# Kernel optimization log

Measured on AMD Instinct MI355X. Metric: run time of the kernel, lower is better.

The kernel has to match this reference:

```python
import jax, jax.numpy as jnp
import numpy as np

EPS = 1e-5
DILATIONS = (1, 2, 1, 2, 1, 2, 1, 2)   # 4 blocks x 2 layers, kernel_size=2
GCN_AT = {1: 0, 5: 1}                  # ChebConv applied before layers 1 and 5
N_NODES, T_IN, N_EDGES = 20000, 13, 200000
RC, DC, SC, EC, HORIZON = 32, 32, 256, 512, 12


def conv_1x1(x, W, b):
    # x: [N,C,T], W: [O,C] -> [N,O,T]
    return jnp.einsum('oc,nct->not', W, x) + b[None, :, None]


def conv_k2(x, W, b, d):
    # dilated conv, kernel=2, dilation=d. x: [N,C,T], W: [O,C,2] -> [N,O,T-d]
    y = jnp.einsum('oc,nct->not', W[:, :, 0], x[:, :, :-d]) \
        + jnp.einsum('oc,nct->not', W[:, :, 1], x[:, :, d:])
    return y + b[None, :, None]


def _batchnorm(x):
    # BatchNorm2d (train mode, gamma=1, beta=0); per-channel stats over (N, F=1, T)
    m = jnp.mean(x, axis=(0, 2), keepdims=True)
    v = jnp.var(x, axis=(0, 2), keepdims=True)
    return (x - m) / jnp.sqrt(v + EPS)


def _cheb(xf, edge_index, edge_attr, W0, W1, b):
    n = xf.shape[0]
    row, col = edge_index[0], edge_index[1]
    w = jnp.where(row == col, 0.0, edge_attr)               # remove_self_loops
    deg = jax.ops.segment_sum(w, row, num_segments=n)
    dinv = jnp.where(deg > 0, 1.0 / jnp.sqrt(jnp.where(deg > 0, deg, 1.0)), 0.0)
    norm = dinv[row] * w * dinv[col]                        # [E]
    tx1 = -jax.ops.segment_sum(norm[:, None] * xf[row], col, num_segments=n)
    return xf @ W0 + tx1 @ W1 + b


def _forward(x, edge_index, edge_attr, start_W, start_b, filter_W, filter_b,
             gate_W, gate_b, skip_W, skip_b, gcn0_W0, gcn0_W1, gcn0_b,
             gcn1_W0, gcn1_W1, gcn1_b, end1_W, end1_b, end2_W, end2_b):
    # instance norm over time (use_norm=True); means is detached in torch
    means = jax.lax.stop_gradient(jnp.mean(x, axis=1, keepdims=True))   # [N,1,1]
    xc = x - means
    stdev = jnp.sqrt(jnp.var(xc, axis=1, keepdims=True) + EPS)
    xc = xc / stdev
    h = xc[:, :, 0][:, None, :]                  # [N,1,13]  (F=1 dim folded away)
    h = conv_1x1(h, start_W, start_b)            # [N,32,13]; T == receptive_field, no pad
    gcns = ((gcn0_W0, gcn0_W1, gcn0_b), (gcn1_W0, gcn1_W1, gcn1_b))
    skip = None
    for i, d in enumerate(DILATIONS):
        if i in GCN_AT:
            n, c, t = h.shape
            W0, W1, b = gcns[GCN_AT[i]]
            h = _cheb(h.reshape(n, c * t), edge_index, edge_attr, W0, W1, b).reshape(n, c, t)
        residual = h
        f = jnp.tanh(conv_k2(residual, filter_W[i], filter_b[i], d))
        g = jax.nn.sigmoid(conv_k2(residual, gate_W[i], gate_b[i], d))
        h = f * g                                 # [N,32,t-d]
        s = conv_1x1(h, skip_W[i], skip_b[i])     # [N,256,t-d]
        skip = s if skip is None else s + skip[:, :, -s.shape[2]:]
        h = h + residual[:, :, -h.shape[2]:]      # residual add (residual_conv unused in source)
        h = _batchnorm(h)
    out = jax.nn.relu(skip)                       # [N,256,1]
    out = conv_1x1(out, end1_W, end1_b)           # [N,512,1]
    out = conv_1x1(out, end2_W, end2_b)           # [N,12,1]
    return out * stdev + means                    # de-normalize; broadcasts over horizon


def setup_inputs() -> dict:
    key = jax.random.key(0)
    ks = iter(jax.random.split(key, 32))
    def w(shape, scale=0.1):
        return jax.random.normal(next(ks), shape, dtype=jnp.float32) * scale
    return {
        'x': jax.random.normal(next(ks), (N_NODES, T_IN, 1), dtype=jnp.float32),
        'edge_index': jax.random.randint(next(ks), (2, N_EDGES), 0, N_NODES),
        'edge_attr': jax.random.uniform(next(ks), (N_EDGES,), dtype=jnp.float32),
        'start_W': w((RC, 1)), 'start_b': w((RC,)),
        'filter_W': w((8, DC, RC, 2)), 'filter_b': w((8, DC)),
        'gate_W': w((8, DC, RC, 2)), 'gate_b': w((8, DC)),
        'skip_W': w((8, SC, DC)), 'skip_b': w((8, SC)),
        'gcn0_W0': w((384, 384), 0.05), 'gcn0_W1': w((384, 384), 0.05), 'gcn0_b': w((384,)),
        'gcn1_W0': w((192, 192), 0.05), 'gcn1_W1': w((192, 192), 0.05), 'gcn1_b': w((192,)),
        'end1_W': w((EC, SC)), 'end1_b': w((EC,)),
        'end2_W': w((HORIZON, EC)), 'end2_b': w((HORIZON,)),
    }


def reference(x, edge_index, edge_attr, start_W, start_b, filter_W, filter_b,
              gate_W, gate_b, skip_W, skip_b, gcn0_W0, gcn0_W1, gcn0_b,
              gcn1_W0, gcn1_W1, gcn1_b, end1_W, end1_b, end2_W, end2_b):
    return _forward(x, edge_index, edge_attr, start_W, start_b, filter_W, filter_b,
                    gate_W, gate_b, skip_W, skip_b, gcn0_W0, gcn0_W1, gcn0_b,
                    gcn1_W0, gcn1_W1, gcn1_b, end1_W, end1_b, end2_W, end2_b)
```

## Files before the change

kernel.cpp:

```cpp
#include <hip/hip_runtime.h>
#include <math.h>

#define NN 20000
#define NE 200000
#define TT 13
#define NBLK 79

typedef short bf16x8 __attribute__((ext_vector_type(8)));
typedef float f32x4 __attribute__((ext_vector_type(4)));

__device__ inline unsigned short f2bf(float f){
  union{float f; unsigned u;} v; v.f = f;
  unsigned r = v.u + 0x7fffu + ((v.u >> 16) & 1u);
  return (unsigned short)(r >> 16);
}
__device__ inline float bf2f(unsigned short h){
  union{unsigned u; float f;} v; v.u = ((unsigned)h) << 16; return v.f;
}
__device__ inline float fsig(float x){ return __builtin_amdgcn_rcpf(1.f + __expf(-x)); }
__device__ inline float ftanh(float x){ return 2.f*__builtin_amdgcn_rcpf(1.f + __expf(-2.f*x)) - 1.f; }

__device__ inline void d_prepw2(const float* W0, const float* W1, const float* b,
    unsigned short* Wt, float* bPerm, int F, int Kp, int T, int idx){
  if(idx >= F*Kp) return;
  int o = idx / Kp, k = idx - o*Kp;
  int to = o >> 5, co = o & 31; int fout = co*T + to;
  int ki = (k < F) ? k : k - F;
  int ti = ki >> 5, ci = ki & 31; int fin = ci*T + ti;
  float v = (k < F) ? W0[fin*F + fout] : W1[fin*F + fout];
  Wt[idx] = f2bf(v);
  if(k == 0) bPerm[o] = b[fout];
}
__device__ inline void d_prep2(const float* sW, const float* sb,
    unsigned short* Bwt, float* b2, int idx){
  if(idx >= 65536) return;
  int sOut = idx >> 8; int ic = idx & 255; int i = ic >> 5; int c = ic & 31;
  Bwt[idx] = f2bf(sW[i*8192 + sOut*32 + c]);
  if(idx < 256){
    float acc = 0.f;
    for(int ll = 0; ll < 8; ll++) acc += sb[ll*256 + idx];
    b2[idx] = acc;
  }
}
__device__ inline void d_comb(const float* e1W, const float* e1b,
    const float* e2W, const float* e2b, float* Wc, float* bc, int idx){
  if(idx >= 12*256) return;
  int k = idx >> 8, c = idx & 255;
  float acc = 0.f;
  for(int o = 0; o < 512; o++) acc += e2W[k*512+o]*e1W[o*256+c];
  Wc[idx] = acc;
  if(c == 0){
    float b = e2b[k];
    for(int o = 0; o < 512; o++) b += e2W[k*512+o]*e1b[o];
    bc[k] = b;
  }
}
__device__ inline void d_prepg(const float* fW, const float* fb,
    const float* gW, const float* gb, unsigned short* Wfrag, float* Bfrag, int idx){
  if(idx < 8*8*64*8){
    int j = idx & 7; int lane = (idx >> 3) & 63; int chunk = (idx >> 9) & 7; int layer = idx >> 12;
    int fg = chunk >> 2; int q = (chunk >> 1) & 1; int i = chunk & 1;
    int quad = lane >> 4, tcol = lane & 15;
    int cout = 16*i + tcol, cin = quad*8 + j;
    const float* W = fg ? gW : fW;
    Wfrag[idx] = f2bf(W[layer*2048 + cout*64 + cin*2 + q]);
  }
  if(idx < 8*64*4){
    int r = idx & 3; int lane = (idx >> 2) & 63; int layer = idx >> 8;
    int tcol = lane & 15;
    float v;
    if(r == 0)      v = fb[layer*32 + tcol];
    else if(r == 1) v = fb[layer*32 + 16 + tcol];
    else if(r == 2) v = gb[layer*32 + tcol];
    else            v = gb[layer*32 + 16 + tcol];
    Bfrag[idx] = v;
  }
}
__global__ __launch_bounds__(256) void k_prepall(
    const float* g0W0, const float* g0W1, const float* g0b,
    const float* g1W0, const float* g1W1, const float* g1b,
    const float* sW, const float* sb,
    const float* e1W, const float* e1b, const float* e2W, const float* e2b,
    const float* fW, const float* fb, const float* gW, const float* gb,
    unsigned short* Wt0, float* bP0, unsigned short* Wt1, float* bP1,
    unsigned short* Bwt, float* bias2, float* Wc, float* bc,
    unsigned short* Wfrag, float* Bfrag){
  int b = blockIdx.x, t = threadIdx.x;
  if(b < 1152)       d_prepw2(g0W0, g0W1, g0b, Wt0, bP0, 384, 768, 12, b*256 + t);
  else if(b < 1440)  d_prepw2(g1W0, g1W1, g1b, Wt1, bP1, 192, 384, 6, (b-1152)*256 + t);
  else if(b < 1696)  d_prep2(sW, sb, Bwt, bias2, (b-1440)*256 + t);
  else if(b < 1708)  d_comb(e1W, e1b, e2W, e2b, Wc, bc, (b-1696)*256 + t);
  else               d_prepg(fW, fb, gW, gb, Wfrag, Bfrag, (b-1708)*256 + t);
}

__global__ __launch_bounds__(256) void k_deg(const int* __restrict__ ei,
    const float* __restrict__ ea, float* __restrict__ deg){
  int e = blockIdx.x*256 + threadIdx.x;
  if(e >= NE) return;
  int r = ei[e], c = ei[NE+e];
  float w = (r==c) ? 0.f : ea[e];
  if(w != 0.f) atomicAdd(&deg[r], w);
}

__global__ __launch_bounds__(256) void k_dinv(float* __restrict__ deg){
  int n = blockIdx.x*256 + threadIdx.x;
  if(n >= NN) return;
  float d = deg[n];
  deg[n] = (d > 0.f) ? rsqrtf(d) : 0.f;
}

__global__ __launch_bounds__(256) void k_normcount(const int* __restrict__ ei,
    const float* __restrict__ ea, const float* __restrict__ dinv,
    float* __restrict__ nrm, int* __restrict__ cnt){
  int e = blockIdx.x*256 + threadIdx.x;
  if(e >= NE) return;
  int r = ei[e], c = ei[NE+e];
  float w = (r==c) ? 0.f : ea[e];
  float nv = dinv[r]*w*dinv[c];
  nrm[e] = nv;
  if(nv != 0.f) atomicAdd(&cnt[c], 1);
}

__global__ __launch_bounds__(256) void k_scanA(const int* __restrict__ cnt, int* __restrict__ bsum){
  int i = blockIdx.x*256 + threadIdx.x;
  int l = threadIdx.x & 63, w = threadIdx.x >> 6;
  int v = (i < NN) ? cnt[i] : 0;
#pragma unroll
  for(int off = 1; off < 64; off <<= 1) v += __shfl_xor(v, off);
  __shared__ int ws4[4];
  if(l == 0) ws4[w] = v;
  __syncthreads();
  if(threadIdx.x == 0) bsum[blockIdx.x] = ws4[0]+ws4[1]+ws4[2]+ws4[3];
}

__global__ __launch_bounds__(128) void k_scanB(const int* __restrict__ bsum, int* __restrict__ bbase){
  __shared__ int buf[128];
  int t = threadIdx.x;
  int v = (t < NBLK) ? bsum[t] : 0;
  buf[t] = v; __syncthreads();
  for(int off = 1; off < 128; off <<= 1){
    int u = (t >= off) ? buf[t-off] : 0;
    __syncthreads();
    buf[t] += u;
    __syncthreads();
  }
  if(t < NBLK) bbase[t] = buf[t] - v;
  if(t == NBLK-1) bbase[NBLK] = buf[t];
}

__global__ __launch_bounds__(256) void k_scanC(const int* __restrict__ cnt,
    const int* __restrict__ bbase, int* __restrict__ rowptr, int* __restrict__ woff){
  int i = blockIdx.x*256 + threadIdx.x;
  int t = threadIdx.x, l = t & 63, w = t >> 6;
  int v = (i < NN) ? cnt[i] : 0;
  int x = v;
#pragma unroll
  for(int off = 1; off < 64; off <<= 1){
    int u = __shfl_up(x, off);
    if(l >= off) x += u;
  }
  __shared__ int wt[4];
  if(l == 63) wt[w] = x;
  __syncthreads();
  int wo = 0;
  for(int k = 0; k < w; k++) wo += wt[k];
  int excl = bbase[blockIdx.x] + wo + x - v;
  if(i < NN){ rowptr[i] = excl; woff[i] = excl; }
  if(i == 0) rowptr[NN] = bbase[NBLK];
}

__global__ __launch_bounds__(256) void k_place(const float* __restrict__ nrm,
    const int* __restrict__ ei, int* __restrict__ woff,
    int* __restrict__ rowArr, float* __restrict__ nrmArr){
  int e = blockIdx.x*256 + threadIdx.x;
  if(e >= NE) return;
  float nv = nrm[e];
  if(nv == 0.f) return;
  int c = ei[NE+e];
  int pos = atomicAdd(&woff[c], 1);
  rowArr[pos] = ei[e];
  nrmArr[pos] = nv;
}

__global__ __launch_bounds__(64) void k_bnfold(const float* __restrict__ in, float* __restrict__ out){
  int t = threadIdx.x;
  float s = 0.f;
#pragma unroll
  for(int b = 0; b < 16; b++) s += in[b*64 + t];
  out[t] = s;
}

__global__ __launch_bounds__(256) void k_cvtbn2(const unsigned short* __restrict__ h,
    const float* __restrict__ bn, float cntInv, unsigned short* __restrict__ A,
    int F, int Kp){
  int idx = blockIdx.x*256 + threadIdx.x;
  int half = F >> 1;
  if(idx >= NN*half) return;
  int n = idx / half, r = idx - n*half;
  int k0 = 2*r; int c0 = k0 & 31;
  unsigned u = *(const unsigned*)(h + (size_t)n*F + k0);
  float m0 = bn[c0]*cntInv, m1 = bn[c0+1]*cntInv;
  float i0 = rsqrtf(bn[32+c0]*cntInv - m0*m0 + 1e-5f);
  float i1 = rsqrtf(bn[32+c0+1]*cntInv - m1*m1 + 1e-5f);
  float v0 = (bf2f((unsigned short)(u & 0xffffu)) - m0)*i0;
  float v1 = (bf2f((unsigned short)(u >> 16)) - m1)*i1;
  unsigned outw = (unsigned)f2bf(v0) | ((unsigned)f2bf(v1) << 16);
  *(unsigned*)(A + (size_t)n*Kp + k0) = outw;
}

__global__ void k_gather2(const unsigned short* __restrict__ Acat, int Kp, int F, int F2,
    const int* __restrict__ rowArr, const float* __restrict__ nrmArr,
    const int* __restrict__ rowptr, unsigned short* __restrict__ dst){
  int node = blockIdx.x;
  int f2 = threadIdx.x;
  int beg = rowptr[node], end = rowptr[node+1];
  __shared__ int srow[64];
  __shared__ float snrm[64];
  float a0 = 0.f, a1 = 0.f;
  for(int base = beg; base < end; base += 64){
    int m = end - base; if(m > 64) m = 64;
    __syncthreads();
    if(threadIdx.x < m){ srow[threadIdx.x] = rowArr[base+threadIdx.x]; snrm[threadIdx.x] = nrmArr[base+threadIdx.x]; }
    __syncthreads();
    if(f2 < F2){
      for(int j = 0; j < m; j++){
        unsigned u = *(const unsigned*)(Acat + (size_t)srow[j]*Kp + 2*f2);
        float nv = snrm[j];
        a0 += nv*bf2f((unsigned short)(u & 0xffffu));
        a1 += nv*bf2f((unsigned short)(u >> 16));
      }
    }
  }
  if(f2 < F2){
    unsigned outw = (unsigned)f2bf(-a0) | ((unsigned)f2bf(-a1) << 16);
    *(unsigned*)(dst + (size_t)node*Kp + F + 2*f2) = outw;
  }
}

template<bool BOUT>
__global__ __launch_bounds__(256) void k_gemm_bf16(const unsigned short* __restrict__ A,
    const unsigned short* __restrict__ Bt, const float* __restrict__ bias,
    void* __restrict__ Cv, int M, int N, int K){
  __shared__ unsigned short As[128*32];
  __shared__ unsigned short Bs[64*32];
  int tid = threadIdx.x;
  int w = tid >> 6, l = tid & 63, quad = l >> 4, tcol = l & 15;
  int m0 = blockIdx.x*128, n0 = blockIdx.y*64;
  int rw = (w & 1)*64, cw = (w >> 1)*32;
  int sr = tid >> 2, sc = (tid & 3)*8;
  f32x4 acc[4][2];
#pragma unroll
  for(int i = 0; i < 4; i++)
#pragma unroll
    for(int j = 0; j < 2; j++) acc[i][j] = (f32x4){0.f,0.f,0.f,0.f};
  for(int k0 = 0; k0 < K; k0 += 32){
    uint4 a0 = *(const uint4*)(A + (size_t)(m0 + sr)*K + k0 + sc);
    uint4 a1 = *(const uint4*)(A + (size_t)(m0 + 64 + sr)*K + k0 + sc);
    uint4 b0 = *(const uint4*)(Bt + (size_t)(n0 + sr)*K + k0 + sc);
    __syncthreads();
    *(uint4*)(As + sr*32 + sc) = a0;
    *(uint4*)(As + (64+sr)*32 + sc) = a1;
    *(uint4*)(Bs + sr*32 + sc) = b0;
    __syncthreads();
    bf16x8 av[4], bv[2];
#pragma unroll
    for(int i = 0; i < 4; i++) av[i] = *(const bf16x8*)(As + (rw + 16*i + tcol)*32 + quad*8);
#pragma unroll
    for(int j = 0; j < 2; j++) bv[j] = *(const bf16x8*)(Bs + (cw + 16*j + tcol)*32 + quad*8);
#pragma unroll
    for(int i = 0; i < 4; i++)
#pragma unroll
      for(int j = 0; j < 2; j++)
        acc[i][j] = __builtin_amdgcn_mfma_f32_16x16x32_bf16(av[i], bv[j], acc[i][j], 0, 0, 0);
  }
#pragma unroll
  for(int i = 0; i < 4; i++){
#pragma unroll
    for(int j = 0; j < 2; j++){
      int col = n0 + cw + 16*j + tcol;
      float bb = bias[col];
#pragma unroll
      for(int r = 0; r < 4; r++){
        int row = m0 + rw + 16*i + quad*4 + r;
        if(row < M){
          float o = acc[i][j][r] + bb;
          if(BOUT) ((unsigned short*)Cv)[(size_t)row*N + col] = f2bf(o);
          else ((float*)Cv)[(size_t)row*N + col] = o;
        }
      }
    }
  }
}

__global__ __launch_bounds__(256,3) void k_fused0nb(
    const float* __restrict__ x, const float* __restrict__ startW, const float* __restrict__ startb,
    const unsigned short* __restrict__ Wfrag, const float* __restrict__ Bfrag,
    unsigned short* __restrict__ glcat, unsigned short* __restrict__ hOut,
    float* __restrict__ stdev, float* __restrict__ means,
    float* __restrict__ bnstats){
  __shared__ float xs[40][14];
  __shared__ float swl[32], sbl[32];
  __shared__ unsigned short bufB[40*12*40];
  __shared__ float bnred[64];
  int tid = threadIdx.x;
  int w = tid >> 6, l = tid & 63, quad = l >> 4, tcol = l & 15;
  int base = blockIdx.x*40;
  for(int j = tid; j < 520; j += 256){ int n = j/13, t = j - n*13; xs[n][t] = x[(size_t)(base+n)*13 + t]; }
  if(tid < 32){ swl[tid] = startW[tid]; sbl[tid] = startb[tid]; }
  if(tid < 64) bnred[tid] = 0.f;
  __syncthreads();
  if(tid < 40){
    float s = 0.f;
#pragma unroll
    for(int t = 0; t < 13; t++) s += xs[tid][t];
    float m = s*(1.0f/13.f);
    float s2 = 0.f;
#pragma unroll
    for(int t = 0; t < 13; t++){ float d = xs[tid][t]-m; s2 += d*d; }
    float sd = sqrtf(s2*(1.0f/13.f) + 1e-5f);
    float inv = 1.0f/sd;
    means[base+tid] = m; stdev[base+tid] = sd;
#pragma unroll
    for(int t = 0; t < 13; t++) xs[tid][t] = (xs[tid][t]-m)*inv;
  }
  __syncthreads();
  bf16x8 bwf[2][2], bwg[2][2];
#pragma unroll
  for(int q = 0; q < 2; q++)
#pragma unroll
    for(int i = 0; i < 2; i++){
      bwf[q][i] = *(const bf16x8*)(Wfrag + ((q*2+i)*64 + l)*8);
      bwg[q][i] = *(const bf16x8*)(Wfrag + ((4 + q*2+i)*64 + l)*8);
    }
  float4 bv4 = *(const float4*)(Bfrag + l*4);
  float fbv[2] = {bv4.x, bv4.y}, gbv[2] = {bv4.z, bv4.w};
  float sw8[8], sb8[8], swc[2], sbc[2];
#pragma unroll
  for(int j = 0; j < 8; j++){ sw8[j] = swl[quad*8+j]; sb8[j] = sbl[quad*8+j]; }
#pragma unroll
  for(int i = 0; i < 2; i++){ swc[i] = swl[16*i+tcol]; sbc[i] = sbl[16*i+tcol]; }
  float sAc[2] = {0.f,0.f}, s2Ac[2] = {0.f,0.f};
  int tr = (tcol < 12) ? tcol : 0;
  for(int p = 0; p < 5; p++){
    int slA = w*10 + 2*p, slB = slA + 1;
    float x0A = xs[slA][tr], x1A = xs[slA][tr+1];
    float x0B = xs[slB][tr], x1B = xs[slB][tr+1];
    bf16x8 aA0, aA1, aB0, aB1;
#pragma unroll
    for(int j = 0; j < 8; j++){
      aA0[j] = (short)f2bf(sw8[j]*x0A + sb8[j]);
      aA1[j] = (short)f2bf(sw8[j]*x1A + sb8[j]);
      aB0[j] = (short)f2bf(sw8[j]*x0B + sb8[j]);
      aB1[j] = (short)f2bf(sw8[j]*x1B + sb8[j]);
    }
    f32x4 afA[2], agA[2], afB[2], agB[2];
#pragma unroll
    for(int i = 0; i < 2; i++){
      afA[i] = (f32x4){0.f,0.f,0.f,0.f}; agA[i] = afA[i];
      afB[i] = afA[i]; agB[i] = afA[i];
    }
#pragma unroll
    for(int i = 0; i < 2; i++){
      afA[i] = __builtin_amdgcn_mfma_f32_16x16x32_bf16(aA0, bwf[0][i], afA[i], 0,0,0);
      afB[i] = __builtin_amdgcn_mfma_f32_16x16x32_bf16(aB0, bwf[0][i], afB[i], 0,0,0);
      afA[i] = __builtin_amdgcn_mfma_f32_16x16x32_bf16(aA1, bwf[1][i], afA[i], 0,0,0);
      afB[i] = __builtin_amdgcn_mfma_f32_16x16x32_bf16(aB1, bwf[1][i], afB[i], 0,0,0);
      agA[i] = __builtin_amdgcn_mfma_f32_16x16x32_bf16(aA0, bwg[0][i], agA[i], 0,0,0);
      agB[i] = __builtin_amdgcn_mfma_f32_16x16x32_bf16(aB0, bwg[0][i], agB[i], 0,0,0);
      agA[i] = __builtin_amdgcn_mfma_f32_16x16x32_bf16(aA1, bwg[1][i], agA[i], 0,0,0);
      agB[i] = __builtin_amdgcn_mfma_f32_16x16x32_bf16(aB1, bwg[1][i], agB[i], 0,0,0);
    }
#pragma unroll
    for(int i = 0; i < 2; i++){
      int cout = 16*i + tcol;
#pragma unroll
      for(int r = 0; r < 4; r++){
        int t = quad*4 + r;
        if(t < 12){
          float fA = afA[i][r] + fbv[i], gA = agA[i][r] + gbv[i];
          float fB = afB[i][r] + fbv[i], gB = agB[i][r] + gbv[i];
          float gatA = ftanh(fA)*fsig(gA);
          float gatB = ftanh(fB)*fsig(gB);
          if(t == 11){
            glcat[(size_t)(base+slA)*256 + cout] = f2bf(gatA);
            glcat[(size_t)(base+slB)*256 + cout] = f2bf(gatB);
          }
          float oA = gatA + swc[i]*xs[slA][t+1] + sbc[i];
          float oB = gatB + swc[i]*xs[slB][t+1] + sbc[i];
          bufB[slA*480 + t*40 + cout] = f2bf(oA);
          bufB[slB*480 + t*40 + cout] = f2bf(oB);
          sAc[i] += oA + oB; s2Ac[i] += oA*oA + oB*oB;
        }
      }
    }
  }
#pragma unroll
  for(int i = 0; i < 2; i++){
    sAc[i]  += __shfl_xor(sAc[i], 16);  sAc[i]  += __shfl_xor(sAc[i], 32);
    s2Ac[i] += __shfl_xor(s2Ac[i], 16); s2Ac[i] += __shfl_xor(s2Ac[i], 32);
  }
  if(l < 16){
#pragma unroll
    for(int i = 0; i < 2; i++){
      atomicAdd(&bnred[16*i + l], sAc[i]);
      atomicAdd(&bnred[32 + 16*i + l], s2Ac[i]);
    }
  }
  __syncthreads();
  if(tid < 64) atomicAdd(&bnstats[(blockIdx.x & 15)*64 + tid], bnred[tid]);
  for(int j = tid; j < 40*48; j += 256){
    int s = j/48; int q = j - s*48; int t = q >> 2; int cb = (q & 3)*8;
    *(uint4*)(hOut + (size_t)(base+s)*384 + t*32 + cb) = *(const uint4*)(bufB + s*480 + t*40 + cb);
  }
}

template<int D,int TIN,int TOUT,bool BNIN,bool STATS,bool WRITEH>
__global__ __launch_bounds__(256) void k_gated5(
    const unsigned short* __restrict__ hIn, unsigned short* __restrict__ hOut,
    unsigned short* __restrict__ gl,
    const float* __restrict__ bnIn, float* __restrict__ bnOut,
    const unsigned short* __restrict__ Wfrag, const float* __restrict__ Bfrag,
    int layer, float cntInv){
  constexpr int RS = 40;
  __shared__ unsigned short hs[4][2][TIN*RS];
  __shared__ unsigned short ho[4][2][WRITEH ? TOUT*RS : RS];
  __shared__ float bnm[32], bnv[32];
  __shared__ float bnred[64];
  int tid = threadIdx.x;
  int w = tid >> 6, l = tid & 63, quad = l >> 4, tcol = l & 15;
  if(BNIN && tid < 32){
    float s = 0.f, s2 = 0.f;
#pragma unroll
    for(int b = 0; b < 16; b++){ s += bnIn[b*64 + tid]; s2 += bnIn[b*64 + 32 + tid]; }
    float m = s*cntInv;
    float var = s2*cntInv - m*m;
    bnm[tid] = m; bnv[tid] = rsqrtf(var + 1e-5f);
  }
  if(STATS && tid < 64) bnred[tid] = 0.f;
  __syncthreads();
  float sm[8], sv[8];
  if(BNIN){
    int cb = (l & 3)*8;
#pragma unroll
    for(int j=0;j<8;j++){ sm[j] = bnm[cb+j]; sv[j] = bnv[cb+j]; }
  }
  const unsigned short* wfr = Wfrag + layer*4096;
  bf16x8 bwf[2][2], bwg[2][2];
#pragma unroll
  for(int q=0;q<2;q++)
#pragma unroll
    for(int i=0;i<2;i++){
      bwf[q][i] = *(const bf16x8*)(wfr + ((q*2+i)*64 + l)*8);
      bwg[q][i] = *(const bf16x8*)(wfr + ((4 + q*2+i)*64 + l)*8);
    }
  float4 bv4 = *(const float4*)(Bfrag + layer*256 + l*4);
  float fbv[2] = {bv4.x, bv4.y}, gbv[2] = {bv4.z, bv4.w};

  int tr = (tcol < TOUT) ? tcol : 0;
  unsigned short* hwA = hs[w][0];
  unsigned short* hwB = hs[w][1];
  unsigned short* howA = ho[w][0];
  unsigned short* howB = ho[w][1];
  float sA[2] = {0.f,0.f}, s2A[2] = {0.f,0.f};
  int wid = blockIdx.x*4 + w;
  int base = wid*4;
  bool ldact = (l < TIN*4);
  int ts = l >> 2, cb = (l & 3)*8;
  uint4 vA = {0,0,0,0}, vB = {0,0,0,0};
  if(ldact && base < NN){
    vA = *(const uint4*)(hIn + (size_t)base*TIN*32 + l*8);
    vB = *(const uint4*)(hIn + (size_t)(base+1)*TIN*32 + l*8);
  }
  for(int p = 0; p < 2; p++){
    int nA = base + 2*p;
    if(nA >= NN) break;
    int nB = nA + 1;
    if(ldact){
      if(BNIN){
        unsigned short tA[8], tB[8];
        const unsigned short* uA = (const unsigned short*)&vA;
        const unsigned short* uB = (const unsigned short*)&vB;
#pragma unroll
        for(int j=0;j<8;j++){
          tA[j] = f2bf((bf2f(uA[j]) - sm[j])*sv[j]);
          tB[j] = f2bf((bf2f(uB[j]) - sm[j])*sv[j]);
        }
        *(uint4*)(hwA + ts*RS + cb) = *(const uint4*)tA;
        *(uint4*)(hwB + ts*RS + cb) = *(const uint4*)tB;
      } else {
        *(uint4*)(hwA + ts*RS + cb) = vA;
        *(uint4*)(hwB + ts*RS + cb) = vB;
      }
    }
    if(p < 1 && ldact && nA + 2 < NN){
      vA = *(const uint4*)(hIn + (size_t)(nA+2)*TIN*32 + l*8);
      vB = *(const uint4*)(hIn + (size_t)(nA+3)*TIN*32 + l*8);
    }
    bf16x8 aA0 = *(const bf16x8*)(hwA + tr*RS + quad*8);
    bf16x8 aA1 = *(const bf16x8*)(hwA + (tr+D)*RS + quad*8);
    bf16x8 aB0 = *(const bf16x8*)(hwB + tr*RS + quad*8);
    bf16x8 aB1 = *(const bf16x8*)(hwB + (tr+D)*RS + quad*8);
    f32x4 afA[2], agA[2], afB[2], agB[2];
#pragma unroll
    for(int i=0;i<2;i++){
      afA[i] = (f32x4){0.f,0.f,0.f,0.f}; agA[i] = afA[i];
      afB[i] = afA[i]; agB[i] = afA[i];
    }
#pragma unroll
    for(int i=0;i<2;i++){
      afA[i] = __builtin_amdgcn_mfma_f32_16x16x32_bf16(aA0, bwf[0][i], afA[i], 0,0,0);
      afB[i] = __builtin_amdgcn_mfma_f32_16x16x32_bf16(aB0, bwf[0][i], afB[i], 0,0,0);
      afA[i] = __builtin_amdgcn_mfma_f32_16x16x32_bf16(aA1, bwf[1][i], afA[i], 0,0,0);
      afB[i] = __builtin_amdgcn_mfma_f32_16x16x32_bf16(aB1, bwf[1][i], afB[i], 0,0,0);
      agA[i] = __builtin_amdgcn_mfma_f32_16x16x32_bf16(aA0, bwg[0][i], agA[i], 0,0,0);
      agB[i] = __builtin_amdgcn_mfma_f32_16x16x32_bf16(aB0, bwg[0][i], agB[i], 0,0,0);
      agA[i] = __builtin_amdgcn_mfma_f32_16x16x32_bf16(aA1, bwg[1][i], agA[i], 0,0,0);
      agB[i] = __builtin_amdgcn_mfma_f32_16x16x32_bf16(aB1, bwg[1][i], agB[i], 0,0,0);
    }
#pragma unroll
    for(int i=0;i<2;i++){
      int cout = 16*i + tcol;
#pragma unroll
      for(int r=0;r<4;r++){
        int t = quad*4 + r;
        if(t < TOUT){
          float fA = afA[i][r] + fbv[i];
          float gA = agA[i][r] + gbv[i];
          float fB = afB[i][r] + fbv[i];
          float gB = agB[i][r] + gbv[i];
          float gatedA = ftanh(fA)*fsig(gA);
          float gatedB = ftanh(fB)*fsig(gB);
          if(t == TOUT-1){
            gl[(size_t)nA*256 + cout] = f2bf(gatedA);
            gl[(size_t)nB*256 + cout] = f2bf(gatedB);
          }
          float oA = gatedA + bf2f(hwA[(t+D)*RS + cout]);
          float oB = gatedB + bf2f(hwB[(t+D)*RS + cout]);
          if(WRITEH){ howA[t*RS + cout] = f2bf(oA); howB[t*RS + cout] = f2bf(oB); }
          if(STATS){ sA[i] += oA + oB; s2A[i] += oA*oA + oB*oB; }
        }
      }
    }
    if(WRITEH && l < TOUT*4){
      int to = l >> 2, cb2 = (l & 3)*8;
      *(uint4*)(hOut + (size_t)nA*TOUT*32 + to*32 + cb2) = *(const uint4*)(howA + to*RS + cb2);
      *(uint4*)(hOut + (size_t)nB*TOUT*32 + to*32 + cb2) = *(const uint4*)(howB + to*RS + cb2);
    }
  }
  if(STATS){
#pragma unroll
    for(int i=0;i<2;i++){
      sA[i]  += __shfl_xor(sA[i], 16);  sA[i]  += __shfl_xor(sA[i], 32);
      s2A[i] += __shfl_xor(s2A[i], 16); s2A[i] += __shfl_xor(s2A[i], 32);
    }
    if(l < 16){
#pragma unroll
      for(int i=0;i<2;i++){
        atomicAdd(&bnred[16*i + l], sA[i]);
        atomicAdd(&bnred[32 + 16*i + l], s2A[i]);
      }
    }
    __syncthreads();
    if(tid < 64) atomicAdd(&bnOut[(blockIdx.x & 15)*64 + tid], bnred[tid]);
  }
}

__global__ __launch_bounds__(256) void k_final(const float* __restrict__ skip,
    const float* __restrict__ Wc, const float* __restrict__ bc,
    const float* __restrict__ stdev, const float* __restrict__ means,
    float* __restrict__ out){
  __shared__ float wsm[3072];
  __shared__ float bcs[12];
  int tid = threadIdx.x;
  for(int j = tid; j < 3072; j += 256){
    int c = j / 12, k = j - c*12;
    wsm[c*12 + k] = Wc[k*256 + c];
  }
  if(tid < 12) bcs[tid] = bc[tid];
  __syncthreads();
  int idx = blockIdx.x*256 + tid;
  if(idx >= NN*12) return;
  int n = idx / 12, k = idx - n*12;
  const float* sr = skip + (size_t)n*256;
  float acc = bcs[k];
#pragma unroll 8
  for(int c = 0; c < 256; c++) acc += wsm[c*12 + k]*fmaxf(sr[c], 0.f);
  out[idx] = acc*stdev[n] + means[n];
}

extern "C" void kernel_launch(void* const* d_in, const int* in_sizes, int n_in,
                              void* d_out, int out_size, void* d_ws, size_t ws_size,
                              hipStream_t stream) {
  const float* x      = (const float*)d_in[0];
  const int*   ei     = (const int*)  d_in[1];
  const float* ea     = (const float*)d_in[2];
  const float* startW = (const float*)d_in[3];
  const float* startb = (const float*)d_in[4];
  const float* fW     = (const float*)d_in[5];
  const float* fb     = (const float*)d_in[6];
  const float* gW     = (const float*)d_in[7];
  const float* gb     = (const float*)d_in[8];
  const float* sW     = (const float*)d_in[9];
  const float* sb     = (const float*)d_in[10];
  const float* g0W0   = (const float*)d_in[11];
  const float* g0W1   = (const float*)d_in[12];
  const float* g0b    = (const float*)d_in[13];
  const float* g1W0   = (const float*)d_in[14];
  const float* g1W1   = (const float*)d_in[15];
  const float* g1b    = (const float*)d_in[16];
  const float* e1W    = (const float*)d_in[17];
  const float* e1b    = (const float*)d_in[18];
  const float* e2W    = (const float*)d_in[19];
  const float* e2b    = (const float*)d_in[20];
  float* out = (float*)d_out;
  float* ws  = (float*)d_ws;

  const int MP = 20096;
  size_t o = 0;
  float* hAf = ws + o; o += (size_t)NN*208;
  float* hBf = ws + o; o += (size_t)NN*208;
  unsigned short* hA = (unsigned short*)hAf;
  unsigned short* hB = (unsigned short*)hBf;
  unsigned short* Acat  = (unsigned short*)(ws + o); o += (size_t)MP*384;
  unsigned short* glcat = (unsigned short*)(ws + o); o += (size_t)MP*128;
  unsigned short* Wt0 = (unsigned short*)(ws + o); o += 147456;
  unsigned short* Wt1 = (unsigned short*)(ws + o); o += 36864;
  unsigned short* Bwt = (unsigned short*)(ws + o); o += 32768;
  unsigned short* Wfrag = (unsigned short*)(ws + o); o += 16384;
  float* Bfrag = ws + o; o += 2048;
  float* bP0   = ws + o; o += 384;
  float* bP1   = ws + o; o += 192;
  float* bias2 = ws + o; o += 256;
  float* Wc    = ws + o; o += 3072;
  float* bc    = ws + o; o += 16;
  float* stdev = ws + o; o += NN;
  float* means = ws + o; o += NN;
  float* deg   = ws + o; o += NN;
  int*   cnt   = (int*)(ws + o); o += NN;
  float* bnstats = ws + o; o += 8*1024;
  float* bnf0  = ws + o; o += 64;
  float* bnf1  = ws + o; o += 64;
  float* normb = ws + o; o += NE;
  int*   rowArr = (int*)(ws + o); o += NE;
  float* nrmArr = ws + o; o += NE;
  int*   rowptr = (int*)(ws + o); o += NN + 4;
  int*   woff   = (int*)(ws + o); o += NN;
  int*   bsum   = (int*)(ws + o); o += NBLK + 4;
  int*   bbase  = (int*)(ws + o); o += NBLK + 4;
  float* skipb  = hAf;

  hipMemsetAsync(deg, 0, (size_t)(2*NN + 8*1024)*sizeof(float), stream);
  k_prepall<<<1836, 256, 0, stream>>>(g0W0, g0W1, g0b, g1W0, g1W1, g1b,
      sW, sb, e1W, e1b, e2W, e2b, fW, fb, gW, gb,
      Wt0, bP0, Wt1, bP1, Bwt, bias2, Wc, bc, Wfrag, Bfrag);
  k_deg<<<(NE+255)/256, 256, 0, stream>>>(ei, ea, deg);
  k_dinv<<<(NN+255)/256, 256, 0, stream>>>(deg);
  k_normcount<<<(NE+255)/256, 256, 0, stream>>>(ei, ea, deg, normb, cnt);
  k_scanA<<<NBLK, 256, 0, stream>>>(cnt, bsum);
  k_scanB<<<1, 128, 0, stream>>>(bsum, bbase);
  k_scanC<<<NBLK, 256, 0, stream>>>(cnt, bbase, rowptr, woff);
  k_place<<<(NE+255)/256, 256, 0, stream>>>(normb, ei, woff, rowArr, nrmArr);

  const int GB = 1280;
  k_fused0nb<<<500, 256, 0, stream>>>(x, startW, startb, Wfrag, Bfrag, glcat, hB,
      stdev, means, bnstats);
  k_bnfold<<<1, 64, 0, stream>>>(bnstats, bnf0);
  k_cvtbn2<<<((NN*192)+255)/256, 256, 0, stream>>>(hB, bnf0, 1.f/(NN*12.f), Acat, 384, 768);
  k_gather2<<<NN, 192, 0, stream>>>(Acat, 768, 384, 192, rowArr, nrmArr, rowptr, Acat);
  { dim3 g(MP/128, 384/64);
    k_gemm_bf16<true><<<g, 256, 0, stream>>>(Acat, Wt0, bP0, hA, NN, 384, 768); }
  k_gated5<2,12,10,false,true,true><<<GB,256,0,stream>>>(hA, hB, glcat+32,
      bnstats, bnstats+1*1024, Wfrag, Bfrag, 1, 0.f);
  k_gated5<1,10,9,true,true,true><<<GB,256,0,stream>>>(hB, hA, glcat+64,
      bnstats+1*1024, bnstats+2*1024, Wfrag, Bfrag, 2, 1.f/(NN*10.f));
  k_gated5<2,9,7,true,true,true><<<GB,256,0,stream>>>(hA, hB, glcat+96,
      bnstats+2*1024, bnstats+3*1024, Wfrag, Bfrag, 3, 1.f/(NN*9.f));
  k_gated5<1,7,6,true,true,true><<<GB,256,0,stream>>>(hB, hA, glcat+128,
      bnstats+3*1024, bnstats+4*1024, Wfrag, Bfrag, 4, 1.f/(NN*7.f));
  k_bnfold<<<1, 64, 0, stream>>>(bnstats+4*1024, bnf1);
  k_cvtbn2<<<((NN*96)+255)/256, 256, 0, stream>>>(hA, bnf1, 1.f/(NN*6.f), Acat, 192, 384);
  k_gather2<<<NN, 128, 0, stream>>>(Acat, 384, 192, 96, rowArr, nrmArr, rowptr, Acat);
  { dim3 g(MP/128, 192/64);
    k_gemm_bf16<true><<<g, 256, 0, stream>>>(Acat, Wt1, bP1, hB, NN, 192, 384); }
  k_gated5<2,6,4,false,true,true><<<GB,256,0,stream>>>(hB, hA, glcat+160,
      bnstats, bnstats+5*1024, Wfrag, Bfrag, 5, 0.f);
  k_gated5<1,4,3,true,true,true><<<GB,256,0,stream>>>(hA, hB, glcat+192,
      bnstats+5*1024, bnstats+6*1024, Wfrag, Bfrag, 6, 1.f/(NN*4.f));
  k_gated5<2,3,1,true,false,false><<<GB,256,0,stream>>>(hB, nullptr, glcat+224,
      bnstats+6*1024, bnstats+7*1024, Wfrag, Bfrag, 7, 1.f/(NN*3.f));

  { dim3 g(MP/128, 256/64);
    k_gemm_bf16<false><<<g, 256, 0, stream>>>(glcat, Bwt, bias2, skipb, NN, 256, 256); }
  k_final<<<((NN*12)+255)/256, 256, 0, stream>>>(skipb, Wc, bc, stdev, means, out);
}
```

Before: 440.9 us.

## Fuse batchnorm fold/apply into gather and GCN GEMM, merge scan kernels

```diff
diff --git a/kernel.cpp b/kernel.cpp
--- a/kernel.cpp
+++ b/kernel.cpp
@@ -133,25 +133,21 @@
   if(threadIdx.x == 0) bsum[blockIdx.x] = ws4[0]+ws4[1]+ws4[2]+ws4[3];
 }
 
-__global__ __launch_bounds__(128) void k_scanB(const int* __restrict__ bsum, int* __restrict__ bbase){
-  __shared__ int buf[128];
+__global__ __launch_bounds__(256) void k_scanC(const int* __restrict__ cnt,
+    const int* __restrict__ bsum, int* __restrict__ rowptr, int* __restrict__ woff){
+  __shared__ int sb[128];
   int t = threadIdx.x;
-  int v = (t < NBLK) ? bsum[t] : 0;
-  buf[t] = v; __syncthreads();
+  if(t < 128) sb[t] = (t < NBLK) ? bsum[t] : 0;
+  __syncthreads();
   for(int off = 1; off < 128; off <<= 1){
-    int u = (t >= off) ? buf[t-off] : 0;
-    __syncthreads();
-    buf[t] += u;
-    __syncthreads();
-  }
-  if(t < NBLK) bbase[t] = buf[t] - v;
-  if(t == NBLK-1) bbase[NBLK] = buf[t];
-}
-
-__global__ __launch_bounds__(256) void k_scanC(const int* __restrict__ cnt,
-    const int* __restrict__ bbase, int* __restrict__ rowptr, int* __restrict__ woff){
-  int i = blockIdx.x*256 + threadIdx.x;
-  int t = threadIdx.x, l = t & 63, w = t >> 6;
+    int u = 0;
+    if(t < 128 && t >= off) u = sb[t-off];
+    __syncthreads();
+    if(t < 128) sb[t] += u;
+    __syncthreads();
+  }
+  int i = blockIdx.x*256 + t;
+  int l = t & 63, w = t >> 6;
   int v = (i < NN) ? cnt[i] : 0;
   int x = v;
 #pragma unroll
@@ -164,9 +160,10 @@
   __syncthreads();
   int wo = 0;
   for(int k = 0; k < w; k++) wo += wt[k];
-  int excl = bbase[blockIdx.x] + wo + x - v;
+  int bb = (blockIdx.x > 0) ? sb[blockIdx.x-1] : 0;
+  int excl = bb + wo + x - v;
   if(i < NN){ rowptr[i] = excl; woff[i] = excl; }
-  if(i == 0) rowptr[NN] = bbase[NBLK];
+  if(i == 0) rowptr[NN] = sb[NBLK-1];
 }
 
 __global__ __launch_bounds__(256) void k_place(const float* __restrict__ nrm,
@@ -182,58 +179,130 @@
   nrmArr[pos] = nv;
 }
 
-__global__ __launch_bounds__(64) void k_bnfold(const float* __restrict__ in, float* __restrict__ out){
-  int t = threadIdx.x;
-  float s = 0.f;
-#pragma unroll
-  for(int b = 0; b < 16; b++) s += in[b*64 + t];
-  out[t] = s;
-}
-
-__global__ __launch_bounds__(256) void k_cvtbn2(const unsigned short* __restrict__ h,
-    const float* __restrict__ bn, float cntInv, unsigned short* __restrict__ A,
-    int F, int Kp){
-  int idx = blockIdx.x*256 + threadIdx.x;
-  int half = F >> 1;
-  if(idx >= NN*half) return;
-  int n = idx / half, r = idx - n*half;
-  int k0 = 2*r; int c0 = k0 & 31;
-  unsigned u = *(const unsigned*)(h + (size_t)n*F + k0);
-  float m0 = bn[c0]*cntInv, m1 = bn[c0+1]*cntInv;
-  float i0 = rsqrtf(bn[32+c0]*cntInv - m0*m0 + 1e-5f);
-  float i1 = rsqrtf(bn[32+c0+1]*cntInv - m1*m1 + 1e-5f);
-  float v0 = (bf2f((unsigned short)(u & 0xffffu)) - m0)*i0;
-  float v1 = (bf2f((unsigned short)(u >> 16)) - m1)*i1;
-  unsigned outw = (unsigned)f2bf(v0) | ((unsigned)f2bf(v1) << 16);
-  *(unsigned*)(A + (size_t)n*Kp + k0) = outw;
-}
-
-__global__ void k_gather2(const unsigned short* __restrict__ Acat, int Kp, int F, int F2,
+__global__ void k_gather3(const unsigned short* __restrict__ h, int F, int F2,
+    const float* __restrict__ bnstats, float cntInv,
     const int* __restrict__ rowArr, const float* __restrict__ nrmArr,
-    const int* __restrict__ rowptr, unsigned short* __restrict__ dst){
-  int node = blockIdx.x;
-  int f2 = threadIdx.x;
-  int beg = rowptr[node], end = rowptr[node+1];
+    const int* __restrict__ rowptr, unsigned short* __restrict__ tx1){
+  __shared__ float bnm[32], bnv[32];
   __shared__ int srow[64];
   __shared__ float snrm[64];
+  int tid = threadIdx.x;
+  if(tid < 32){
+    float s = 0.f, s2 = 0.f;
+#pragma unroll
+    for(int b = 0; b < 16; b++){ s += bnstats[b*64 + tid]; s2 += bnstats[b*64 + 32 + tid]; }
+    float m = s*cntInv; float var = s2*cntInv - m*m;
+    bnm[tid] = m; bnv[tid] = rsqrtf(var + 1e-5f);
+  }
+  __syncthreads();
+  int node = blockIdx.x;
+  int f2 = tid;
+  int c0 = (2*f2) & 31;
+  float m0 = bnm[c0], i0 = bnv[c0], m1 = bnm[c0+1], i1 = bnv[c0+1];
+  int beg = rowptr[node], end = rowptr[node+1];
   float a0 = 0.f, a1 = 0.f;
   for(int base = beg; base < end; base += 64){
     int m = end - base; if(m > 64) m = 64;
     __syncthreads();
-    if(threadIdx.x < m){ srow[threadIdx.x] = rowArr[base+threadIdx.x]; snrm[threadIdx.x] = nrmArr[base+threadIdx.x]; }
+    if(tid < m){ srow[tid] = rowArr[base+tid]; snrm[tid] = nrmArr[base+tid]; }
     __syncthreads();
     if(f2 < F2){
       for(int j = 0; j < m; j++){
-        unsigned u = *(const unsigned*)(Acat + (size_t)srow[j]*Kp + 2*f2);
+        unsigned u = *(const unsigned*)(h + (size_t)srow[j]*F + 2*f2);
         float nv = snrm[j];
-        a0 += nv*bf2f((unsigned short)(u & 0xffffu));
-        a1 += nv*bf2f((unsigned short)(u >> 16));
+        a0 += nv*(bf2f((unsigned short)(u & 0xffffu)) - m0)*i0;
+        a1 += nv*(bf2f((unsigned short)(u >> 16)) - m1)*i1;
       }
     }
   }
   if(f2 < F2){
     unsigned outw = (unsigned)f2bf(-a0) | ((unsigned)f2bf(-a1) << 16);
-    *(unsigned*)(dst + (size_t)node*Kp + F + 2*f2) = outw;
+    *(unsigned*)(tx1 + (size_t)node*F + 2*f2) = outw;
+  }
+}
+
+template<bool BOUT>
+__global__ __launch_bounds__(256) void k_gemm_gcn(
+    const unsigned short* __restrict__ hSrc, const unsigned short* __restrict__ tx1,
+    const unsigned short* __restrict__ Bt, const float* __restrict__ bias,
+    const float* __restrict__ bnstats, float cntInv,
+    void* __restrict__ Cv, int M, int N, int F){
+  __shared__ unsigned short As[128*32];
+  __shared__ unsigned short Bs[64*32];
+  __shared__ float bnm[32], bnv[32];
+  int tid = threadIdx.x;
+  if(tid < 32){
+    float s = 0.f, s2 = 0.f;
+#pragma unroll
+    for(int b = 0; b < 16; b++){ s += bnstats[b*64 + tid]; s2 += bnstats[b*64 + 32 + tid]; }
+    float m = s*cntInv; float var = s2*cntInv - m*m;
+    bnm[tid] = m; bnv[tid] = rsqrtf(var + 1e-5f);
+  }
+  __syncthreads();
+  int w = tid >> 6, l = tid & 63, quad = l >> 4, tcol = l & 15;
+  int m0 = blockIdx.x*128, n0 = blockIdx.y*64;
+  int rw = (w & 1)*64, cw = (w >> 1)*32;
+  int sr = tid >> 2, sc = (tid & 3)*8;
+  float am[8], ai[8];
+#pragma unroll
+  for(int j = 0; j < 8; j++){ am[j] = bnm[sc+j]; ai[j] = bnv[sc+j]; }
+  int K = 2*F;
+  f32x4 acc[4][2];
+#pragma unroll
+  for(int i = 0; i < 4; i++)
+#pragma unroll
+    for(int j = 0; j < 2; j++) acc[i][j] = (f32x4){0.f,0.f,0.f,0.f};
+  for(int k0 = 0; k0 < K; k0 += 32){
+    uint4 a0r, a1r;
+    if(k0 < F){
+      uint4 r0 = *(const uint4*)(hSrc + (size_t)(m0 + sr)*F + k0 + sc);
+      uint4 r1 = *(const uint4*)(hSrc + (size_t)(m0 + 64 + sr)*F + k0 + sc);
+      unsigned short o0[8], o1[8];
+      const unsigned short* p0 = (const unsigned short*)&r0;
+      const unsigned short* p1 = (const unsigned short*)&r1;
+#pragma unroll
+      for(int j = 0; j < 8; j++){
+        o0[j] = f2bf((bf2f(p0[j]) - am[j])*ai[j]);
+        o1[j] = f2bf((bf2f(p1[j]) - am[j])*ai[j]);
+      }
+      a0r = *(const uint4*)o0; a1r = *(const uint4*)o1;
+    } else {
+      a0r = *(const uint4*)(tx1 + (size_t)(m0 + sr)*F + (k0-F) + sc);
+      a1r = *(const uint4*)(tx1 + (size_t)(m0 + 64 + sr)*F + (k0-F) + sc);
+    }
+    uint4 b0 = *(const uint4*)(Bt + (size_t)(n0 + sr)*K + k0 + sc);
+    __syncthreads();
+    *(uint4*)(As + sr*32 + sc) = a0r;
+    *(uint4*)(As + (64+sr)*32 + sc) = a1r;
+    *(uint4*)(Bs + sr*32 + sc) = b0;
+    __syncthreads();
+    bf16x8 av[4], bv[2];
+#pragma unroll
+    for(int i = 0; i < 4; i++) av[i] = *(const bf16x8*)(As + (rw + 16*i + tcol)*32 + quad*8);
+#pragma unroll
+    for(int j = 0; j < 2; j++) bv[j] = *(const bf16x8*)(Bs + (cw + 16*j + tcol)*32 + quad*8);
+#pragma unroll
+    for(int i = 0; i < 4; i++)
+#pragma unroll
+      for(int j = 0; j < 2; j++)
+        acc[i][j] = __builtin_amdgcn_mfma_f32_16x16x32_bf16(av[i], bv[j], acc[i][j], 0, 0, 0);
+  }
+#pragma unroll
+  for(int i = 0; i < 4; i++){
+#pragma unroll
+    for(int j = 0; j < 2; j++){
+      int col = n0 + cw + 16*j + tcol;
+      float bb = bias[col];
+#pragma unroll
+      for(int r = 0; r < 4; r++){
+        int row = m0 + rw + 16*i + quad*4 + r;
+        if(row < M){
+          float o = acc[i][j][r] + bb;
+          if(BOUT) ((unsigned short*)Cv)[(size_t)row*N + col] = f2bf(o);
+          else ((float*)Cv)[(size_t)row*N + col] = o;
+        }
+      }
+    }
   }
 }
 
@@ -621,7 +690,7 @@
   float* hBf = ws + o; o += (size_t)NN*208;
   unsigned short* hA = (unsigned short*)hAf;
   unsigned short* hB = (unsigned short*)hBf;
-  unsigned short* Acat  = (unsigned short*)(ws + o); o += (size_t)MP*384;
+  unsigned short* tx1   = (unsigned short*)(ws + o); o += (size_t)MP*192;
   unsigned short* glcat = (unsigned short*)(ws + o); o += (size_t)MP*128;
   unsigned short* Wt0 = (unsigned short*)(ws + o); o += 147456;
   unsigned short* Wt1 = (unsigned short*)(ws + o); o += 36864;
@@ -638,15 +707,12 @@
   float* deg   = ws + o; o += NN;
   int*   cnt   = (int*)(ws + o); o += NN;
   float* bnstats = ws + o; o += 8*1024;
-  float* bnf0  = ws + o; o += 64;
-  float* bnf1  = ws + o; o += 64;
   float* normb = ws + o; o += NE;
   int*   rowArr = (int*)(ws + o); o += NE;
   float* nrmArr = ws + o; o += NE;
   int*   rowptr = (int*)(ws + o); o += NN + 4;
   int*   woff   = (int*)(ws + o); o += NN;
   int*   bsum   = (int*)(ws + o); o += NBLK + 4;
-  int*   bbase  = (int*)(ws + o); o += NBLK + 4;
   float* skipb  = hAf;
 
   hipMemsetAsync(deg, 0, (size_t)(2*NN + 8*1024)*sizeof(float), stream);
@@ -657,18 +723,17 @@
   k_dinv<<<(NN+255)/256, 256, 0, stream>>>(deg);
   k_normcount<<<(NE+255)/256, 256, 0, stream>>>(ei, ea, deg, normb, cnt);
   k_scanA<<<NBLK, 256, 0, stream>>>(cnt, bsum);
-  k_scanB<<<1, 128, 0, stream>>>(bsum, bbase);
-  k_scanC<<<NBLK, 256, 0, stream>>>(cnt, bbase, rowptr, woff);
+  k_scanC<<<NBLK, 256, 0, stream>>>(cnt, bsum, rowptr, woff);
   k_place<<<(NE+255)/256, 256, 0, stream>>>(normb, ei, woff, rowArr, nrmArr);
 
   const int GB = 1280;
   k_fused0nb<<<500, 256, 0, stream>>>(x, startW, startb, Wfrag, Bfrag, glcat, hB,
       stdev, means, bnstats);
-  k_bnfold<<<1, 64, 0, stream>>>(bnstats, bnf0);
-  k_cvtbn2<<<((NN*192)+255)/256, 256, 0, stream>>>(hB, bnf0, 1.f/(NN*12.f), Acat, 384, 768);
-  k_gather2<<<NN, 192, 0, stream>>>(Acat, 768, 384, 192, rowArr, nrmArr, rowptr, Acat);
+  k_gather3<<<NN, 192, 0, stream>>>(hB, 384, 192, bnstats, 1.f/(NN*12.f),
+      rowArr, nrmArr, rowptr, tx1);
   { dim3 g(MP/128, 384/64);
-    k_gemm_bf16<true><<<g, 256, 0, stream>>>(Acat, Wt0, bP0, hA, NN, 384, 768); }
+    k_gemm_gcn<true><<<g, 256, 0, stream>>>(hB, tx1, Wt0, bP0, bnstats, 1.f/(NN*12.f),
+        hA, NN, 384, 384); }
   k_gated5<2,12,10,false,true,true><<<GB,256,0,stream>>>(hA, hB, glcat+32,
       bnstats, bnstats+1*1024, Wfrag, Bfrag, 1, 0.f);
   k_gated5<1,10,9,true,true,true><<<GB,256,0,stream>>>(hB, hA, glcat+64,
@@ -677,11 +742,11 @@
       bnstats+2*1024, bnstats+3*1024, Wfrag, Bfrag, 3, 1.f/(NN*9.f));
   k_gated5<1,7,6,true,true,true><<<GB,256,0,stream>>>(hB, hA, glcat+128,
       bnstats+3*1024, bnstats+4*1024, Wfrag, Bfrag, 4, 1.f/(NN*7.f));
-  k_bnfold<<<1, 64, 0, stream>>>(bnstats+4*1024, bnf1);
-  k_cvtbn2<<<((NN*96)+255)/256, 256, 0, stream>>>(hA, bnf1, 1.f/(NN*6.f), Acat, 192, 384);
-  k_gather2<<<NN, 128, 0, stream>>>(Acat, 384, 192, 96, rowArr, nrmArr, rowptr, Acat);
+  k_gather3<<<NN, 128, 0, stream>>>(hA, 192, 96, bnstats+4*1024, 1.f/(NN*6.f),
+      rowArr, nrmArr, rowptr, tx1);
   { dim3 g(MP/128, 192/64);
-    k_gemm_bf16<true><<<g, 256, 0, stream>>>(Acat, Wt1, bP1, hB, NN, 192, 384); }
+    k_gemm_gcn<true><<<g, 256, 0, stream>>>(hA, tx1, Wt1, bP1, bnstats+4*1024, 1.f/(NN*6.f),
+        hB, NN, 192, 192); }
   k_gated5<2,6,4,false,true,true><<<GB,256,0,stream>>>(hB, hA, glcat+160,
       bnstats, bnstats+5*1024, Wfrag, Bfrag, 5, 0.f);
   k_gated5<1,4,3,true,true,true><<<GB,256,0,stream>>>(hA, hB, glcat+192,
```

New measurement: 432.8 us. No clear change (-1.8%).
